# Kernel tuning notes

Hardware: AMD Instinct MI355X
Metric: run time of the kernel (lower is better)

## Reference

```python
import jax, jax.numpy as jnp
import numpy as np

N, MAX_DEG, F_IN, F_OUT = 20000, 32, 128, 128
TRIM_RATIO = 0.45
N_NEIGH_THRESHOLD = 3


def setup_inputs() -> dict:
    key = jax.random.key(0)
    k_h, k_nbr, k_deg, k_w, k_b = jax.random.split(key, 5)
    h = jax.random.normal(k_h, (N, F_IN), dtype=jnp.float32)
    nbr = jax.random.randint(k_nbr, (N, MAX_DEG), 0, N, dtype=jnp.int32)
    # in-degree in [1, MAX_DEG] so every node has at least one neighbor
    deg = jax.random.randint(k_deg, (N,), 1, MAX_DEG + 1, dtype=jnp.int32)
    # GCN symmetric normalizer deg^-0.5, per node, shape [N, 1]
    norm = (deg.astype(jnp.float32) ** -0.5)[:, None]
    stdv = 1.0 / np.sqrt(F_OUT)
    weight = jax.random.uniform(k_w, (F_IN, F_OUT), jnp.float32, -stdv, stdv)
    bias = jax.random.uniform(k_b, (F_OUT,), jnp.float32, -stdv, stdv)
    return {"h": h, "norm": norm, "weight": weight, "bias": bias,
            "nbr": nbr, "deg": deg}


def reference(h, norm, weight, bias, nbr, deg):
    # h: [N,F] node features (dropout=0 so input_ft == dropped_h == h)
    # nbr: [N,D] padded src indices; deg: [N] valid neighbor counts; norm: [N,1]
    D = nbr.shape[1]
    slot = jnp.arange(D, dtype=deg.dtype)[None, :]            # [1,D]
    valid = slot < deg[:, None]                                # [N,D]

    h_nbr = h[nbr]                                             # [N,D,F] = mailbox input_ft
    msg = h_nbr * norm[nbr]                                    # [N,D,F] = mailbox m (src h * src norm)

    # padded slots -> +inf so they sort past all valid entries (ranks >= deg)
    big = jnp.asarray(jnp.finfo(h.dtype).max, h.dtype)
    ift = jnp.where(valid[..., None], h_nbr, big)
    sidx = jnp.argsort(ift, axis=1)                            # per-feature sort over neighbors
    gathered = jnp.take_along_axis(msg, sidx, axis=1)          # [N,D,F]

    n = deg                                                    # per-node n_neigh
    b_raw = n // 2 - (1 - n % 2)
    b_cap = jnp.floor(n.astype(jnp.float32) * TRIM_RATIO).astype(n.dtype)
    b = jnp.maximum(jnp.minimum(b_raw, b_cap), 1)              # trim count per node

    # keep sorted ranks in [b, n-b)
    sel = (slot >= b[:, None]) & (slot < (n - b)[:, None])     # [N,D]
    trimmed_sum = jnp.sum(gathered * sel[..., None].astype(h.dtype), axis=1)  # [N,F]

    self0 = h * norm                                           # dst h * dst norm (mailbox 'self'[:,0])
    alpha = (2 * b).astype(h.dtype)[:, None]
    accum_med = (trimmed_sum + self0 * alpha) * norm           # trim_compensate=True branch
    accum_small = (n.astype(h.dtype)[:, None] * self0) * norm  # n_neigh <= threshold branch
    accum = jnp.where((n <= N_NEIGH_THRESHOLD)[:, None], accum_small, accum_med)

    # NodeApplyModule_V2: linear + bias + relu
    out = jax.nn.relu(accum @ weight + bias)
    return out
```

## Files before the change

kernel.cpp:

```cpp
#include <hip/hip_runtime.h>
#include <hip/hip_fp16.h>
#include <cfloat>
#include <cmath>

#define N_NODES 20000
#define MAXD 32
#define F 128

#define MTILE 32
#define NBLK (N_NODES / MTILE)

typedef _Float16 half8 __attribute__((ext_vector_type(8)));
typedef float f32x4 __attribute__((ext_vector_type(4)));
typedef unsigned int u32x4 __attribute__((ext_vector_type(4)));
typedef unsigned short us8v __attribute__((ext_vector_type(8)));


template <int SZ, int NV>
__device__ __forceinline__ void oe_sort_n(float (&a)[SZ]) {
#pragma unroll
  for (int p = 1; p < SZ; p <<= 1) {
#pragma unroll
    for (int q = p; q >= 1; q >>= 1) {
#pragma unroll
      for (int j = q % p; j <= SZ - 1 - q; j += 2 * q) {
#pragma unroll
        for (int i = 0; i < q; ++i) {
          int x = i + j, y = i + j + q;
          if (y < NV && (x / (2 * p)) == (y / (2 * p))) {
            float mn = fminf(a[x], a[y]);
            float mx = fmaxf(a[x], a[y]);
            a[x] = mn;
            a[y] = mx;
          }
        }
      }
    }
  }
}

template <int N>
struct TrimB {
  static constexpr int b_raw = N / 2 - (1 - (N & 1));
  static constexpr int b_cap = (int)((float)N * 0.45f);
  static constexpr int b_min = b_raw < b_cap ? b_raw : b_cap;
  static constexpr int value = b_min > 1 ? b_min : 1;
};

template <int SZ, int N>
__device__ __forceinline__ float trimmed_sum_n(const float* __restrict__ h,
                                               const float* __restrict__ norm,
                                               const int* __restrict__ nbr_row,
                                               int f) {
  constexpr int B = TrimB<N>::value;
  constexpr int NB = N - B;

  float ko[SZ];
  float nrm[SZ];
  float k[SZ];
#pragma unroll
  for (int d = 0; d < N; ++d) {
    int src = nbr_row[d];
    nrm[d] = norm[src];
    ko[d] = h[src * F + f];
    k[d] = ko[d];
  }
#pragma unroll
  for (int d = N; d < SZ; ++d) k[d] = FLT_MAX;

  oe_sort_n<SZ, N>(k);

  const float lo  = k[B];
  const float hi  = k[NB - 1];
  const float lom = k[B - 1];
  const float him = k[NB];

  float sum = 0.f;
  if ((lom < lo) & (hi < him)) {
#pragma unroll
    for (int d = 0; d < N; ++d) {
      bool keep = (ko[d] >= lo) & (ko[d] <= hi);
      sum = fmaf(keep ? ko[d] : 0.f, nrm[d], sum);
    }
  } else {
    int c_lt_lo = 0, c_lt_hi = 0;
#pragma unroll
    for (int d = 0; d < N; ++d) {
      c_lt_lo += (ko[d] < lo) ? 1 : 0;
      c_lt_hi += (ko[d] < hi) ? 1 : 0;
    }
    int run_lo = 0, run_hi = 0;
#pragma unroll
    for (int d = 0; d < N; ++d) {
      const float kd = ko[d];
      const float m = kd * nrm[d];
      const bool eql = (kd == lo);
      const bool eqh = (kd == hi);
      const bool lh = (lo < hi);
      const bool btw = (kd > lo) & (kd < hi);
      const int r_lo = c_lt_lo + run_lo;
      const int r_hi = c_lt_hi + run_hi;
      const bool inc = btw
                     | (eql & (r_lo >= B) & (lh | (r_lo < NB)))
                     | (lh & eqh & (r_hi < NB));
      sum += inc ? m : 0.f;
      run_lo += eql ? 1 : 0;
      run_hi += eqh ? 1 : 0;
    }
  }
  return sum;
}

__device__ __forceinline__ unsigned int split_pack(float v) {
  _Float16 hi = (_Float16)v;
  _Float16 lo = (_Float16)(v - (float)hi);
  unsigned short hb = __builtin_bit_cast(unsigned short, hi);
  unsigned short lb = __builtin_bit_cast(unsigned short, lo);
  return (unsigned int)hb | ((unsigned int)lb << 16);
}

__global__ __launch_bounds__(128) void gcn_stage1(const float* __restrict__ h,
                                                  const float* __restrict__ norm,
                                                  const int* __restrict__ nbr,
                                                  const int* __restrict__ deg,
                                                  const float* __restrict__ W,
                                                  unsigned int* __restrict__ Ap,
                                                  _Float16* __restrict__ Whl) {
  const int i = blockIdx.x;
  const int f = threadIdx.x;

  if (i < 16) {
    const int e0 = (i * 128 + f) * 8;
#pragma unroll
    for (int j = 0; j < 8; ++j) {
      const int e = e0 + j;
      const int k = e >> 7, n = e & 127;
      const float w = W[e];
      const _Float16 whi = (_Float16)w;
      Whl[n * F + k] = whi;
      Whl[16384 + n * F + k] = (_Float16)(w - (float)whi);
    }
  }

  const int n = deg[i];
  const float ni = norm[i];
  const float hif = h[i * F + f];
  const int idx = i * F + f;

  if (n <= 3) {
    Ap[idx] = split_pack((float)n * hif * ni * ni);
    return;
  }

  const int* nbr_row = nbr + i * MAXD;
  float ts;
  int b;
  switch (n) {
#define TS_CASE(NN, SS) \
    case NN: ts = trimmed_sum_n<SS, NN>(h, norm, nbr_row, f); b = TrimB<NN>::value; break;
    TS_CASE(4, 4)
    TS_CASE(5, 8) TS_CASE(6, 8) TS_CASE(7, 8) TS_CASE(8, 8)
    TS_CASE(9, 16) TS_CASE(10, 16) TS_CASE(11, 16) TS_CASE(12, 16)
    TS_CASE(13, 16) TS_CASE(14, 16) TS_CASE(15, 16) TS_CASE(16, 16)
    TS_CASE(17, 32) TS_CASE(18, 32) TS_CASE(19, 32) TS_CASE(20, 32)
    TS_CASE(21, 32) TS_CASE(22, 32) TS_CASE(23, 32) TS_CASE(24, 32)
    TS_CASE(25, 32) TS_CASE(26, 32) TS_CASE(27, 32) TS_CASE(28, 32)
    TS_CASE(29, 32) TS_CASE(30, 32) TS_CASE(31, 32)
    default: ts = trimmed_sum_n<32, 32>(h, norm, nbr_row, f); b = TrimB<32>::value; break;
#undef TS_CASE
  }

  Ap[idx] = split_pack((ts + hif * ni * (float)(2 * b)) * ni);
}

__global__ __launch_bounds__(256) void gcn_gemm_mfma(
    const unsigned int* __restrict__ Ap, const _Float16* __restrict__ Whl,
    const float* __restrict__ bias, float* __restrict__ out) {
  const int t = threadIdx.x;
  const int lane = t & 63;
  const int wv = t >> 6;
  const int l16 = lane & 15;
  const int kg = lane >> 4;
  const int row0 = blockIdx.x * MTILE;
  const int colb = wv * 32;

  f32x4 acc[2][2];
#pragma unroll
  for (int rf = 0; rf < 2; ++rf)
#pragma unroll
    for (int cf = 0; cf < 2; ++cf) acc[rf][cf] = (f32x4){0.f, 0.f, 0.f, 0.f};

#pragma unroll
  for (int kc = 0; kc < F; kc += 32) {
    half8 ah[2], al[2], bh[2], bl[2];
#pragma unroll
    for (int rf = 0; rf < 2; ++rf) {
      const int row = row0 + rf * 16 + l16;
      const unsigned int* p = Ap + (size_t)row * F + kc + kg * 8;
      u32x4 p0 = *(const u32x4*)p;
      u32x4 p1 = *(const u32x4*)(p + 4);
      us8v s0 = __builtin_bit_cast(us8v, p0);
      us8v s1 = __builtin_bit_cast(us8v, p1);
      ah[rf] = __builtin_bit_cast(half8,
          (us8v)__builtin_shufflevector(s0, s1, 0, 2, 4, 6, 8, 10, 12, 14));
      al[rf] = __builtin_bit_cast(half8,
          (us8v)__builtin_shufflevector(s0, s1, 1, 3, 5, 7, 9, 11, 13, 15));
    }
#pragma unroll
    for (int cf = 0; cf < 2; ++cf) {
      const int n = colb + cf * 16 + l16;
      bh[cf] = *(const half8*)(Whl + n * F + kc + kg * 8);
      bl[cf] = *(const half8*)(Whl + 16384 + n * F + kc + kg * 8);
    }
#pragma unroll
    for (int rf = 0; rf < 2; ++rf)
#pragma unroll
      for (int cf = 0; cf < 2; ++cf) {
        acc[rf][cf] = __builtin_amdgcn_mfma_f32_16x16x32_f16(ah[rf], bh[cf], acc[rf][cf], 0, 0, 0);
        acc[rf][cf] = __builtin_amdgcn_mfma_f32_16x16x32_f16(ah[rf], bl[cf], acc[rf][cf], 0, 0, 0);
        acc[rf][cf] = __builtin_amdgcn_mfma_f32_16x16x32_f16(al[rf], bh[cf], acc[rf][cf], 0, 0, 0);
      }
  }

#pragma unroll
  for (int cf = 0; cf < 2; ++cf) {
    const int col = colb + cf * 16 + l16;
    const float bv = bias[col];
#pragma unroll
    for (int rf = 0; rf < 2; ++rf) {
#pragma unroll
      for (int r = 0; r < 4; ++r) {
        const int row = row0 + rf * 16 + kg * 4 + r;
        out[(size_t)row * F + col] = fmaxf(acc[rf][cf][r] + bv, 0.f);
      }
    }
  }
}

extern "C" void kernel_launch(void* const* d_in, const int* in_sizes, int n_in,
                              void* d_out, int out_size, void* d_ws, size_t ws_size,
                              hipStream_t stream) {
  const float* h = (const float*)d_in[0];
  const float* norm = (const float*)d_in[1];
  const float* weight = (const float*)d_in[2];
  const float* bias = (const float*)d_in[3];
  const int* nbr = (const int*)d_in[4];
  const int* deg = (const int*)d_in[5];
  float* out = (float*)d_out;

  unsigned int* Ap = (unsigned int*)d_ws;
  _Float16* Whl = (_Float16*)(Ap + (size_t)N_NODES * F);

  gcn_stage1<<<N_NODES, 128, 0, stream>>>(h, norm, nbr, deg, weight, Ap, Whl);
  gcn_gemm_mfma<<<NBLK, 256, 0, stream>>>(Ap, Whl, bias, out);
}
```

Measured before the change: 112.7 us.

## Fuse trimmed aggregation with MFMA GEMM via swizzled shared-memory tile

Merges the per-node trimmed-mean aggregation and the split-fp16 MFMA GEMM into one kernel. Each 256-thread block aggregates 16 nodes into a XOR-swizzled LDS tile and then multiplies it by the weights, so the global round-trip of the packed intermediate matrix is gone. Weight hi/lo splitting moves to a small separate prep kernel. The trade-off is less parallelism in the aggregation: 1250 blocks each loop over 8 node pairs, instead of 20000 blocks with one node each, which could expose latency from the degree-dependent branches.

```diff
diff --git a/kernel.cpp b/kernel.cpp
--- a/kernel.cpp
+++ b/kernel.cpp
@@ -7,7 +7,7 @@
 #define MAXD 32
 #define F 128
 
-#define MTILE 32
+#define MTILE 16
 #define NBLK (N_NODES / MTILE)
 
 typedef _Float16 half8 __attribute__((ext_vector_type(8)));
@@ -119,107 +119,94 @@
   return (unsigned int)hb | ((unsigned int)lb << 16);
 }
 
-__global__ __launch_bounds__(128) void gcn_stage1(const float* __restrict__ h,
-                                                  const float* __restrict__ norm,
-                                                  const int* __restrict__ nbr,
-                                                  const int* __restrict__ deg,
-                                                  const float* __restrict__ W,
-                                                  unsigned int* __restrict__ Ap,
-                                                  _Float16* __restrict__ Whl) {
-  const int i = blockIdx.x;
-  const int f = threadIdx.x;
-
-  if (i < 16) {
-    const int e0 = (i * 128 + f) * 8;
-#pragma unroll
-    for (int j = 0; j < 8; ++j) {
-      const int e = e0 + j;
-      const int k = e >> 7, n = e & 127;
-      const float w = W[e];
-      const _Float16 whi = (_Float16)w;
-      Whl[n * F + k] = whi;
-      Whl[16384 + n * F + k] = (_Float16)(w - (float)whi);
-    }
-  }
-
-  const int n = deg[i];
-  const float ni = norm[i];
-  const float hif = h[i * F + f];
-  const int idx = i * F + f;
-
-  if (n <= 3) {
-    Ap[idx] = split_pack((float)n * hif * ni * ni);
-    return;
-  }
-
-  const int* nbr_row = nbr + i * MAXD;
-  float ts;
-  int b;
-  switch (n) {
+__global__ __launch_bounds__(256) void whl_prep(const float* __restrict__ W,
+                                                _Float16* __restrict__ Whl) {
+  const int e = blockIdx.x * 256 + threadIdx.x;
+  const int n = e >> 7, k = e & 127;
+  const float w = W[k * F + n];
+  const _Float16 hi = (_Float16)w;
+  Whl[e] = hi;
+  Whl[16384 + e] = (_Float16)(w - (float)hi);
+}
+
+__global__ __launch_bounds__(256) void gcn_fused(
+    const float* __restrict__ h, const float* __restrict__ norm,
+    const int* __restrict__ nbr, const int* __restrict__ deg,
+    const _Float16* __restrict__ Whl, const float* __restrict__ bias,
+    float* __restrict__ out) {
+  __shared__ unsigned int As[MTILE * F];
+  const int tid = threadIdx.x;
+  const int hw = __builtin_amdgcn_readfirstlane(tid) >> 7;
+  const int f = tid & 127;
+
+#pragma unroll 1
+  for (int it = 0; it < 8; ++it) {
+    const int nl = it * 2 + hw;
+    const int i = blockIdx.x * MTILE + nl;
+    const int n = deg[i];
+    const float ni = norm[i];
+    const float hif = h[i * F + f];
+
+    float val;
+    if (n <= 3) {
+      val = (float)n * hif * ni * ni;
+    } else {
+      const int* nbr_row = nbr + i * MAXD;
+      float ts;
+      int b;
+      switch (n) {
 #define TS_CASE(NN, SS) \
-    case NN: ts = trimmed_sum_n<SS, NN>(h, norm, nbr_row, f); b = TrimB<NN>::value; break;
-    TS_CASE(4, 4)
-    TS_CASE(5, 8) TS_CASE(6, 8) TS_CASE(7, 8) TS_CASE(8, 8)
-    TS_CASE(9, 16) TS_CASE(10, 16) TS_CASE(11, 16) TS_CASE(12, 16)
-    TS_CASE(13, 16) TS_CASE(14, 16) TS_CASE(15, 16) TS_CASE(16, 16)
-    TS_CASE(17, 32) TS_CASE(18, 32) TS_CASE(19, 32) TS_CASE(20, 32)
-    TS_CASE(21, 32) TS_CASE(22, 32) TS_CASE(23, 32) TS_CASE(24, 32)
-    TS_CASE(25, 32) TS_CASE(26, 32) TS_CASE(27, 32) TS_CASE(28, 32)
-    TS_CASE(29, 32) TS_CASE(30, 32) TS_CASE(31, 32)
-    default: ts = trimmed_sum_n<32, 32>(h, norm, nbr_row, f); b = TrimB<32>::value; break;
+        case NN: ts = trimmed_sum_n<SS, NN>(h, norm, nbr_row, f); b = TrimB<NN>::value; break;
+        TS_CASE(4, 4)
+        TS_CASE(5, 8) TS_CASE(6, 8) TS_CASE(7, 8) TS_CASE(8, 8)
+        TS_CASE(9, 16) TS_CASE(10, 16) TS_CASE(11, 16) TS_CASE(12, 16)
+        TS_CASE(13, 16) TS_CASE(14, 16) TS_CASE(15, 16) TS_CASE(16, 16)
+        TS_CASE(17, 32) TS_CASE(18, 32) TS_CASE(19, 32) TS_CASE(20, 32)
+        TS_CASE(21, 32) TS_CASE(22, 32) TS_CASE(23, 32) TS_CASE(24, 32)
+        TS_CASE(25, 32) TS_CASE(26, 32) TS_CASE(27, 32) TS_CASE(28, 32)
+        TS_CASE(29, 32) TS_CASE(30, 32) TS_CASE(31, 32)
+        default: ts = trimmed_sum_n<32, 32>(h, norm, nbr_row, f); b = TrimB<32>::value; break;
 #undef TS_CASE
-  }
-
-  Ap[idx] = split_pack((ts + hif * ni * (float)(2 * b)) * ni);
-}
-
-__global__ __launch_bounds__(256) void gcn_gemm_mfma(
-    const unsigned int* __restrict__ Ap, const _Float16* __restrict__ Whl,
-    const float* __restrict__ bias, float* __restrict__ out) {
-  const int t = threadIdx.x;
-  const int lane = t & 63;
-  const int wv = t >> 6;
+      }
+      val = (ts + hif * ni * (float)(2 * b)) * ni;
+    }
+    As[nl * F + (f ^ ((nl & 7) << 2))] = split_pack(val);
+  }
+
+  __syncthreads();
+
+  const int lane = tid & 63;
+  const int wv = tid >> 6;
   const int l16 = lane & 15;
   const int kg = lane >> 4;
   const int row0 = blockIdx.x * MTILE;
   const int colb = wv * 32;
-
-  f32x4 acc[2][2];
-#pragma unroll
-  for (int rf = 0; rf < 2; ++rf)
-#pragma unroll
-    for (int cf = 0; cf < 2; ++cf) acc[rf][cf] = (f32x4){0.f, 0.f, 0.f, 0.f};
+  const int s = (l16 & 7) << 2;
+
+  f32x4 acc[2];
+  acc[0] = (f32x4){0.f, 0.f, 0.f, 0.f};
+  acc[1] = (f32x4){0.f, 0.f, 0.f, 0.f};
 
 #pragma unroll
   for (int kc = 0; kc < F; kc += 32) {
-    half8 ah[2], al[2], bh[2], bl[2];
-#pragma unroll
-    for (int rf = 0; rf < 2; ++rf) {
-      const int row = row0 + rf * 16 + l16;
-      const unsigned int* p = Ap + (size_t)row * F + kc + kg * 8;
-      u32x4 p0 = *(const u32x4*)p;
-      u32x4 p1 = *(const u32x4*)(p + 4);
-      us8v s0 = __builtin_bit_cast(us8v, p0);
-      us8v s1 = __builtin_bit_cast(us8v, p1);
-      ah[rf] = __builtin_bit_cast(half8,
-          (us8v)__builtin_shufflevector(s0, s1, 0, 2, 4, 6, 8, 10, 12, 14));
-      al[rf] = __builtin_bit_cast(half8,
-          (us8v)__builtin_shufflevector(s0, s1, 1, 3, 5, 7, 9, 11, 13, 15));
-    }
+    const int k0 = kc + kg * 8;
+    u32x4 p0 = *(const u32x4*)(As + l16 * F + ((k0 + 0) ^ s));
+    u32x4 p1 = *(const u32x4*)(As + l16 * F + ((k0 + 4) ^ s));
+    us8v s0 = __builtin_bit_cast(us8v, p0);
+    us8v s1 = __builtin_bit_cast(us8v, p1);
+    half8 ah = __builtin_bit_cast(half8,
+        (us8v)__builtin_shufflevector(s0, s1, 0, 2, 4, 6, 8, 10, 12, 14));
+    half8 al = __builtin_bit_cast(half8,
+        (us8v)__builtin_shufflevector(s0, s1, 1, 3, 5, 7, 9, 11, 13, 15));
 #pragma unroll
     for (int cf = 0; cf < 2; ++cf) {
       const int n = colb + cf * 16 + l16;
-      bh[cf] = *(const half8*)(Whl + n * F + kc + kg * 8);
-      bl[cf] = *(const half8*)(Whl + 16384 + n * F + kc + kg * 8);
-    }
-#pragma unroll
-    for (int rf = 0; rf < 2; ++rf)
-#pragma unroll
-      for (int cf = 0; cf < 2; ++cf) {
-        acc[rf][cf] = __builtin_amdgcn_mfma_f32_16x16x32_f16(ah[rf], bh[cf], acc[rf][cf], 0, 0, 0);
-        acc[rf][cf] = __builtin_amdgcn_mfma_f32_16x16x32_f16(ah[rf], bl[cf], acc[rf][cf], 0, 0, 0);
-        acc[rf][cf] = __builtin_amdgcn_mfma_f32_16x16x32_f16(al[rf], bh[cf], acc[rf][cf], 0, 0, 0);
-      }
+      half8 bh = *(const half8*)(Whl + n * F + k0);
+      half8 bl = *(const half8*)(Whl + 16384 + n * F + k0);
+      acc[cf] = __builtin_amdgcn_mfma_f32_16x16x32_f16(ah, bh, acc[cf], 0, 0, 0);
+      acc[cf] = __builtin_amdgcn_mfma_f32_16x16x32_f16(ah, bl, acc[cf], 0, 0, 0);
+      acc[cf] = __builtin_amdgcn_mfma_f32_16x16x32_f16(al, bh, acc[cf], 0, 0, 0);
+    }
   }
 
 #pragma unroll
@@ -227,12 +214,9 @@
     const int col = colb + cf * 16 + l16;
     const float bv = bias[col];
 #pragma unroll
-    for (int rf = 0; rf < 2; ++rf) {
-#pragma unroll
-      for (int r = 0; r < 4; ++r) {
-        const int row = row0 + rf * 16 + kg * 4 + r;
-        out[(size_t)row * F + col] = fmaxf(acc[rf][cf][r] + bv, 0.f);
-      }
+    for (int r = 0; r < 4; ++r) {
+      const int row = row0 + kg * 4 + r;
+      out[(size_t)row * F + col] = fmaxf(acc[cf][r] + bv, 0.f);
     }
   }
 }
@@ -248,9 +232,8 @@
   const int* deg = (const int*)d_in[5];
   float* out = (float*)d_out;
 
-  unsigned int* Ap = (unsigned int*)d_ws;
-  _Float16* Whl = (_Float16*)(Ap + (size_t)N_NODES * F);
-
-  gcn_stage1<<<N_NODES, 128, 0, stream>>>(h, norm, nbr, deg, weight, Ap, Whl);
-  gcn_gemm_mfma<<<NBLK, 256, 0, stream>>>(Ap, Whl, bias, out);
-}
+  _Float16* Whl = (_Float16*)d_ws;
+
+  whl_prep<<<64, 256, 0, stream>>>(weight, Whl);
+  gcn_fused<<<NBLK, 256, 0, stream>>>(h, norm, nbr, deg, Whl, bias, out);
+}
```

Measured after the change: 115.3 us. 1.02x slower.
